# Kernel optimization log

Measured on AMD Instinct MI355X. Metric: run time of the kernel, lower is better.

Reference implementation:

```python
import jax, jax.numpy as jnp
import numpy as np

D_MODEL = 1024
D_FF = 4096


def _layernorm(x, gamma, beta, eps=1e-5):
    mu = jnp.mean(x, axis=-1, keepdims=True)
    var = jnp.var(x, axis=-1, keepdims=True)
    return (x - mu) * jax.lax.rsqrt(var + eps) * gamma + beta


def setup_inputs() -> dict:
    key = jax.random.key(0)
    ks = jax.random.split(key, 7)
    B, S = 4, 2048
    src = jax.random.normal(ks[0], (B, S, D_MODEL), dtype=jnp.float32)
    gamma1 = jnp.ones((D_MODEL,), jnp.float32)
    beta1 = jnp.zeros((D_MODEL,), jnp.float32)
    gamma2 = jnp.ones((D_MODEL,), jnp.float32)
    beta2 = jnp.zeros((D_MODEL,), jnp.float32)
    w1 = jax.random.normal(ks[1], (D_MODEL, D_FF), jnp.float32) * (1.0 / np.sqrt(D_MODEL))
    b1 = jnp.zeros((D_FF,), jnp.float32)
    w2 = jax.random.normal(ks[2], (D_FF, D_MODEL), jnp.float32) * (1.0 / np.sqrt(D_FF))
    b2 = jnp.zeros((D_MODEL,), jnp.float32)
    return {"src": src, "gamma1": gamma1, "beta1": beta1,
            "gamma2": gamma2, "beta2": beta2,
            "w1": w1, "b1": b1, "w2": w2, "b2": b2}


def reference(src, gamma1, beta1, gamma2, beta2, w1, b1, w2, b2):
    # Pre-LN self-attention (single head, Q=K=V=norm_x, no projections)
    norm_x = _layernorm(src, gamma1, beta1)
    dim_k = norm_x.shape[-1]
    scores = jnp.einsum('bqd,bkd->bqk', norm_x, norm_x) / jnp.sqrt(jnp.float32(dim_k))
    weights = jax.nn.softmax(scores, axis=-1)
    attn = jnp.einsum('bqk,bkd->bqd', weights, norm_x)
    x = src + attn  # dropout p=0 -> identity
    # Pre-LN FFN
    h = _layernorm(x, gamma2, beta2)
    h = jax.nn.gelu(h @ w1 + b1, approximate=False)
    h = h @ w2 + b2
    return h + x
```

## Files before the change

kernel.cpp:

```cpp
#include <hip/hip_runtime.h>
#include <hip/hip_bf16.h>
#include <math.h>

typedef __attribute__((ext_vector_type(8))) short s8vec;
typedef __attribute__((ext_vector_type(16))) float f32x16;
typedef __attribute__((ext_vector_type(4))) unsigned short us4;

__device__ __forceinline__ unsigned short f2bf(float f) {
  unsigned u = __float_as_uint(f);
  u = (u + 0x7fffu + ((u >> 16) & 1u)) >> 16;
  return (unsigned short)u;
}
__device__ __forceinline__ float bf2f(unsigned short u) {
  return __uint_as_float(((unsigned)u) << 16);
}

__device__ __forceinline__ float fast_gelu(float t) {
  float t2 = t * t;
  float u = t * (1.59576912f + 0.07135481f * t2);
  float e = __expf(-u);
  return t * __frcp_rn(1.0f + e);
}

__device__ __forceinline__ void async_ld16(const unsigned short* g, unsigned short* l) {
  __builtin_amdgcn_global_load_lds(
      (__attribute__((address_space(1))) void*)g,
      (__attribute__((address_space(3))) void*)l, 16, 0, 0);
}


#define STA(q, tk, bofs) async_ld16(srcA[q] + ((size_t)(tk) << 6), &As[(bofs) + ldsA[q]])
#define STB(j, tk, bofs) async_ld16(srcB[j] + ((size_t)(tk) << 6), &Bs[(bofs) + ldsB[j]])

#define ARD(Q)                                                              \
  _Pragma("unroll") for (int s = 0; s < 4; ++s)                             \
      af[s] = *(const s8vec*)&As[aB + aoff + (Q)*2048 + pc[s]];

#define MFMA_PH(Q)                                                          \
  __builtin_amdgcn_s_barrier();                                             \
  asm volatile("s_waitcnt lgkmcnt(0)" ::: "memory");                        \
  __builtin_amdgcn_sched_barrier(0);                                        \
  __builtin_amdgcn_s_setprio(1);                                            \
  _Pragma("unroll") for (int s = 0; s < 4; ++s) {                           \
    _Pragma("unroll") for (int nf = 0; nf < NF; ++nf)                       \
      acc[Q][nf] = __builtin_amdgcn_mfma_f32_32x32x16_bf16(                 \
          af[s], b[nf][s], acc[Q][nf], 0, 0, 0);                            \
  }                                                                         \
  __builtin_amdgcn_s_setprio(0);

template <int BN, int EPI>
__global__ __launch_bounds__(512, 2) void gemm_nt8(
    const unsigned short* __restrict__ A, const unsigned short* __restrict__ B,
    float* __restrict__ outF, unsigned short* __restrict__ outB,
    const float* __restrict__ bias, const float* __restrict__ res,
    int M, int N, int K,
    long long bA, long long bB, long long bO, long long bR, float scale)
{
  static_assert(BN == 256 || BN == 128, "BN must be 256 or 128");
  constexpr int NB = BN / 64;
  constexpr int NF = BN / 128;
  constexpr int WN = BN / 4;
  constexpr int ABUF = 256 * 64;
  constexpr int BBUF = BN * 64;

  __shared__ __align__(16) unsigned short As[2 * ABUF];
  __shared__ __align__(16) unsigned short Bs[2 * BBUF];

  (void)M;
  const int tid = threadIdx.x;
  const int w = tid >> 6;
  const int l = tid & 63;
  const int z = blockIdx.z;
  A += (size_t)z * bA;
  B += (size_t)z * bB;
  const size_t tileM = (size_t)blockIdx.y * 256;
  const size_t tileN = (size_t)blockIdx.x * BN;

  const int sub = w & 3, half = w >> 2;
  const unsigned short* srcA[4];
  int ldsA[4];
#pragma unroll
  for (int q = 0; q < 4; ++q) {
    const int rb = q * 32 + sub * 8 + half * 128;
    const int r = rb + (l >> 3);
    const int c = (l & 7) ^ (r & 7) ^ ((r >> 3) & 3);
    srcA[q] = A + (tileM + r) * (size_t)K + (c << 3);
    ldsA[q] = rb * 64;
  }
  const unsigned short* srcB[NB];
  int ldsB[NB];
#pragma unroll
  for (int j = 0; j < NB; ++j) {
    const int rb = j * 64 + w * 8;
    const int r = rb + (l >> 3);
    const int c = (l & 7) ^ (r & 7) ^ ((r >> 3) & 3);
    srcB[j] = B + (tileN + r) * (size_t)K + (c << 3);
    ldsB[j] = rb * 64;
  }

  const int wm = half;
  const int wn = sub;
  const int fr = l & 31;
  const int fq = l >> 5;
  const int swz = (l & 7) ^ ((l >> 3) & 3);
  int pc[4];
#pragma unroll
  for (int s = 0; s < 4; ++s) pc[s] = ((((s << 1) + fq) ^ swz) << 3);
  const int aoff = (wm * 128 + fr) * 64;
  int boff[NF];
#pragma unroll
  for (int nf = 0; nf < NF; ++nf) boff[nf] = (wn * WN + nf * 32 + fr) * 64;

  f32x16 acc[4][NF] = {};
  const int NT = K >> 6;

  STA(0, 0, 0); STA(1, 0, 0); STA(2, 0, 0); STA(3, 0, 0);
#pragma unroll
  for (int j = 0; j < NB; ++j) STB(j, 0, 0);
#pragma unroll
  for (int j = 0; j < NB; ++j) STB(j, 1, BBUF);
  STA(0, 1, ABUF); STA(1, 1, ABUF);
  if constexpr (BN == 256) asm volatile("s_waitcnt vmcnt(6)" ::: "memory");
  else                     asm volatile("s_waitcnt vmcnt(4)" ::: "memory");
  __builtin_amdgcn_s_barrier();

  auto tile = [&](int t, int bf) {
    const int aB = bf * ABUF;
    const int bBo = bf * BBUF;
    const int oaB = (bf ^ 1) * ABUF;
    const bool g1 = (t + 1 < NT), g2 = (t + 2 < NT);
    s8vec b[NF][4];
    s8vec af[4];

    ARD(0);
#pragma unroll
    for (int nf = 0; nf < NF; ++nf)
#pragma unroll
      for (int s = 0; s < 4; ++s)
        b[nf][s] = *(const s8vec*)&Bs[bBo + boff[nf] + pc[s]];
    if (g1) { STA(2, t + 1, oaB); STA(3, t + 1, oaB); }
    MFMA_PH(0);
    __builtin_amdgcn_s_barrier();

    ARD(1);
    if (g2) {
      if constexpr (BN == 256) { STB(0, t + 2, bBo); STB(1, t + 2, bBo); }
      else                     { STB(0, t + 2, bBo); }
    }
    MFMA_PH(1);
    __builtin_amdgcn_s_barrier();

    ARD(2);
    if (g2) {
      if constexpr (BN == 256) { STB(2, t + 2, bBo); STB(3, t + 2, bBo); }
      else                     { STB(1, t + 2, bBo); }
    }
    MFMA_PH(2);
    __builtin_amdgcn_s_barrier();

    ARD(3);
    if (g2) { STA(0, t + 2, aB); STA(1, t + 2, aB); }
    MFMA_PH(3);
    if (g2) {
      if constexpr (BN == 256) asm volatile("s_waitcnt vmcnt(6)" ::: "memory");
      else                     asm volatile("s_waitcnt vmcnt(4)" ::: "memory");
    } else {
      asm volatile("s_waitcnt vmcnt(0)" ::: "memory");
    }
    __builtin_amdgcn_s_barrier();
  };

  for (int t = 0; t < NT; t += 2) { tile(t, 0); tile(t + 1, 1); }

  float* oF = outF + (size_t)z * bO;
  unsigned short* oB = outB + (size_t)z * bO;
  const float* rs = res + (size_t)z * bR;

  float bcol[NF];
  if (EPI >= 2) {
#pragma unroll
    for (int nf = 0; nf < NF; ++nf) bcol[nf] = bias[tileN + wn * WN + nf * 32 + fr];
  }

#pragma unroll
  for (int mf = 0; mf < 4; ++mf) {
#pragma unroll
    for (int r = 0; r < 16; ++r) {
      const size_t row = tileM + wm * 128 + (mf << 5) + (r & 3) + ((r >> 2) << 3) + (fq << 2);
      const size_t rb = row * (size_t)N;
#pragma unroll
      for (int nf = 0; nf < NF; ++nf) {
        const size_t col = tileN + wn * WN + (nf << 5) + fr;
        const float v = acc[mf][nf][r];
        if (EPI == 0) {
          oB[rb + col] = f2bf(v * scale);
        } else if (EPI == 1) {
          oF[rb + col] = v + rs[rb + col];
        } else if (EPI == 2) {
          oB[rb + col] = f2bf(fast_gelu(v + bcol[nf]));
        } else {
          oF[rb + col] = v + bcol[nf] + rs[rb + col];
        }
      }
    }
  }
}

__global__ __launch_bounds__(256) void ln_row(
    const float* __restrict__ x, const float* __restrict__ gamma,
    const float* __restrict__ beta, unsigned short* __restrict__ out)
{
  const int row = blockIdx.x;
  const float4* xr = (const float4*)(x + (size_t)row * 1024);
  const int tid = threadIdx.x;
  float4 v = xr[tid];
  float s = v.x + v.y + v.z + v.w;
  float q = v.x * v.x + v.y * v.y + v.z * v.z + v.w * v.w;
#pragma unroll
  for (int off = 32; off > 0; off >>= 1) {
    s += __shfl_down(s, off);
    q += __shfl_down(q, off);
  }
  __shared__ float rs_[4], rq_[4];
  const int w = tid >> 6, l = tid & 63;
  if (l == 0) { rs_[w] = s; rq_[w] = q; }
  __syncthreads();
  s = rs_[0] + rs_[1] + rs_[2] + rs_[3];
  q = rq_[0] + rq_[1] + rq_[2] + rq_[3];
  const float mu = s * (1.0f / 1024.0f);
  const float var = q * (1.0f / 1024.0f) - mu * mu;
  const float rstd = rsqrtf(var + 1e-5f);
  const float4 g = ((const float4*)gamma)[tid];
  const float4 b = ((const float4*)beta)[tid];
  us4 o;
  o.x = f2bf((v.x - mu) * rstd * g.x + b.x);
  o.y = f2bf((v.y - mu) * rstd * g.y + b.y);
  o.z = f2bf((v.z - mu) * rstd * g.z + b.z);
  o.w = f2bf((v.w - mu) * rstd * g.w + b.w);
  ((us4*)(out + (size_t)row * 1024))[tid] = o;
}

__global__ __launch_bounds__(256) void softmax_row(
    const unsigned short* __restrict__ sc, unsigned short* __restrict__ pr)
{
  const int row = blockIdx.x;
  const s8vec* s8 = (const s8vec*)(sc + (size_t)row * 2048);
  const int tid = threadIdx.x;
  s8vec a = s8[tid];
  float x[8];
#pragma unroll
  for (int i = 0; i < 8; ++i) x[i] = bf2f((unsigned short)a[i]);
  float mx = x[0];
#pragma unroll
  for (int i = 1; i < 8; ++i) mx = fmaxf(mx, x[i]);
#pragma unroll
  for (int off = 32; off > 0; off >>= 1) mx = fmaxf(mx, __shfl_down(mx, off));
  __shared__ float red[4];
  const int w = tid >> 6, l = tid & 63;
  if (l == 0) red[w] = mx;
  __syncthreads();
  mx = fmaxf(fmaxf(red[0], red[1]), fmaxf(red[2], red[3]));
  __syncthreads();
  float e[8], s = 0.f;
#pragma unroll
  for (int i = 0; i < 8; ++i) { e[i] = __expf(x[i] - mx); s += e[i]; }
#pragma unroll
  for (int off = 32; off > 0; off >>= 1) s += __shfl_down(s, off);
  if (l == 0) red[w] = s;
  __syncthreads();
  s = red[0] + red[1] + red[2] + red[3];
  const float inv = 1.0f / s;
  s8vec o;
#pragma unroll
  for (int i = 0; i < 8; ++i) o[i] = (short)f2bf(e[i] * inv);
  ((s8vec*)(pr + (size_t)row * 2048))[tid] = o;
}

template <bool BF16IN>
__global__ __launch_bounds__(256) void transpose_conv(
    const void* __restrict__ in_, unsigned short* __restrict__ out,
    int R, int C, long long bIn, long long bOut)
{
  __shared__ float tile[32][33];
  const int z = blockIdx.z;
  const int tx = threadIdx.x, ty = threadIdx.y;
  const int c0 = blockIdx.x * 32, r0 = blockIdx.y * 32;
  if (BF16IN) {
    const unsigned short* in = (const unsigned short*)in_ + (size_t)z * bIn;
    for (int i = ty; i < 32; i += 8)
      tile[i][tx] = bf2f(in[(size_t)(r0 + i) * C + c0 + tx]);
  } else {
    const float* in = (const float*)in_ + (size_t)z * bIn;
    for (int i = ty; i < 32; i += 8)
      tile[i][tx] = in[(size_t)(r0 + i) * C + c0 + tx];
  }
  __syncthreads();
  unsigned short* o = out + (size_t)z * bOut;
  for (int i = ty; i < 32; i += 8)
    o[(size_t)(c0 + i) * R + r0 + tx] = f2bf(tile[tx][i]);
}

extern "C" void kernel_launch(void* const* d_in, const int* in_sizes, int n_in,
                              void* d_out, int out_size, void* d_ws, size_t ws_size,
                              hipStream_t stream)
{
  (void)in_sizes; (void)n_in; (void)out_size; (void)ws_size;
  const float* src = (const float*)d_in[0];
  const float* g1  = (const float*)d_in[1];
  const float* be1 = (const float*)d_in[2];
  const float* g2  = (const float*)d_in[3];
  const float* be2 = (const float*)d_in[4];
  const float* w1  = (const float*)d_in[5];
  const float* b1  = (const float*)d_in[6];
  const float* w2  = (const float*)d_in[7];
  const float* b2  = (const float*)d_in[8];
  float* out = (float*)d_out;

  char* ws = (char*)d_ws;
  const size_t SZ_NORMX  = (size_t)8192 * 1024 * 2;
  const size_t SZ_SCORES = (size_t)4 * 2048 * 2048 * 4;
  const size_t SZ_PROBS  = (size_t)4 * 2048 * 2048 * 2;
  const size_t SZ_X      = (size_t)8192 * 1024 * 4;
  const size_t SZ_W1T    = (size_t)1024 * 4096 * 2;

  unsigned short* normx  = (unsigned short*)(ws);
  unsigned short* normxT = (unsigned short*)(ws + SZ_NORMX);
  unsigned short* scores = (unsigned short*)(ws + 2 * SZ_NORMX);
  unsigned short* probs  = (unsigned short*)(ws + 2 * SZ_NORMX + SZ_SCORES);
  float*          xbuf   = (float*)(ws + 2 * SZ_NORMX + SZ_SCORES + SZ_PROBS);
  unsigned short* w1t    = (unsigned short*)(ws + 2 * SZ_NORMX + SZ_SCORES + SZ_PROBS + SZ_X);
  unsigned short* w2t    = (unsigned short*)(ws + 2 * SZ_NORMX + SZ_SCORES + SZ_PROBS + SZ_X + SZ_W1T);
  unsigned short* normx2 = normx;
  unsigned short* hbuf   = scores;

  const dim3 tb(32, 8);
  transpose_conv<false><<<dim3(128, 32, 1), tb, 0, stream>>>(w1, w1t, 1024, 4096, 0, 0);
  transpose_conv<false><<<dim3(32, 128, 1), tb, 0, stream>>>(w2, w2t, 4096, 1024, 0, 0);

  ln_row<<<8192, 256, 0, stream>>>(src, g1, be1, normx);
  transpose_conv<true><<<dim3(32, 64, 4), tb, 0, stream>>>(
      normx, normxT, 2048, 1024, (long long)2048 * 1024, (long long)1024 * 2048);

  gemm_nt8<256, 0><<<dim3(8, 8, 4), 512, 0, stream>>>(
      normx, normx, nullptr, scores, nullptr, nullptr,
      2048, 2048, 1024,
      (long long)2048 * 1024, (long long)2048 * 1024, (long long)2048 * 2048, 0, 0.03125f);

  softmax_row<<<8192, 256, 0, stream>>>(scores, probs);

  gemm_nt8<128, 1><<<dim3(8, 8, 4), 512, 0, stream>>>(
      probs, normxT, xbuf, nullptr, nullptr, src,
      2048, 1024, 2048,
      (long long)2048 * 2048, (long long)1024 * 2048, (long long)2048 * 1024,
      (long long)2048 * 1024, 1.0f);

  ln_row<<<8192, 256, 0, stream>>>(xbuf, g2, be2, normx2);

  gemm_nt8<256, 2><<<dim3(16, 32, 1), 512, 0, stream>>>(
      normx2, w1t, nullptr, hbuf, b1, nullptr,
      8192, 4096, 1024, 0, 0, 0, 0, 1.0f);

  gemm_nt8<128, 3><<<dim3(8, 32, 1), 512, 0, stream>>>(
      hbuf, w2t, out, nullptr, b2, xbuf,
      8192, 1024, 4096, 0, 0, 0, 0, 1.0f);
}
```

Measured before the change: 429.3 us.

## Remap workgroups across XCDs and restructure BN=128 GEMM loop into two phases

Workgroup indices are remapped so that consecutive tiles land on the same XCD chiplet, to improve L2 locality for shared A/B panels. The BN=128 path now runs two MFMA phases per K-tile, each covering two A fragments, instead of four single-fragment phases. This halves the barriers per K-tile and issues all B and A prefetches together. The remap assumes the grid dims are powers of two and that the workgroup count divides by 8. The new BN=128 schedule also holds more fragments in registers, which may raise register pressure.

```diff
diff --git a/kernel.cpp b/kernel.cpp
--- a/kernel.cpp
+++ b/kernel.cpp
@@ -32,21 +32,15 @@
 #define STA(q, tk, bofs) async_ld16(srcA[q] + ((size_t)(tk) << 6), &As[(bofs) + ldsA[q]])
 #define STB(j, tk, bofs) async_ld16(srcB[j] + ((size_t)(tk) << 6), &Bs[(bofs) + ldsB[j]])
 
-#define ARD(Q)                                                              \
-  _Pragma("unroll") for (int s = 0; s < 4; ++s)                             \
-      af[s] = *(const s8vec*)&As[aB + aoff + (Q)*2048 + pc[s]];
-
-#define MFMA_PH(Q)                                                          \
+#define PH_SYNC_PRE()                                                       \
   __builtin_amdgcn_s_barrier();                                             \
   asm volatile("s_waitcnt lgkmcnt(0)" ::: "memory");                        \
   __builtin_amdgcn_sched_barrier(0);                                        \
-  __builtin_amdgcn_s_setprio(1);                                            \
-  _Pragma("unroll") for (int s = 0; s < 4; ++s) {                           \
-    _Pragma("unroll") for (int nf = 0; nf < NF; ++nf)                       \
-      acc[Q][nf] = __builtin_amdgcn_mfma_f32_32x32x16_bf16(                 \
-          af[s], b[nf][s], acc[Q][nf], 0, 0, 0);                            \
-  }                                                                         \
-  __builtin_amdgcn_s_setprio(0);
+  __builtin_amdgcn_s_setprio(1)
+
+#define PH_SYNC_POST()                                                      \
+  __builtin_amdgcn_s_setprio(0);                                            \
+  __builtin_amdgcn_s_barrier()
 
 template <int BN, int EPI>
 __global__ __launch_bounds__(512, 2) void gemm_nt8(
@@ -70,11 +64,21 @@
   const int tid = threadIdx.x;
   const int w = tid >> 6;
   const int l = tid & 63;
-  const int z = blockIdx.z;
+
+  const unsigned gx = gridDim.x, gy = gridDim.y;
+  unsigned lin = blockIdx.x + gx * (blockIdx.y + gy * blockIdx.z);
+  const unsigned nwg = gx * gy * gridDim.z;
+  lin = (lin & 7u) * (nwg >> 3) + (lin >> 3);
+  const unsigned bx = lin & (gx - 1u);
+  const unsigned tmp = lin >> __builtin_ctz(gx);
+  const unsigned by = tmp & (gy - 1u);
+  const unsigned bz = tmp >> __builtin_ctz(gy);
+
+  const int z = (int)bz;
   A += (size_t)z * bA;
   B += (size_t)z * bB;
-  const size_t tileM = (size_t)blockIdx.y * 256;
-  const size_t tileN = (size_t)blockIdx.x * BN;
+  const size_t tileM = (size_t)by * 256;
+  const size_t tileN = (size_t)bx * BN;
 
   const int sub = w & 3, half = w >> 2;
   const unsigned short* srcA[4];
@@ -114,63 +118,124 @@
   f32x16 acc[4][NF] = {};
   const int NT = K >> 6;
 
-  STA(0, 0, 0); STA(1, 0, 0); STA(2, 0, 0); STA(3, 0, 0);
-#pragma unroll
-  for (int j = 0; j < NB; ++j) STB(j, 0, 0);
-#pragma unroll
-  for (int j = 0; j < NB; ++j) STB(j, 1, BBUF);
-  STA(0, 1, ABUF); STA(1, 1, ABUF);
-  if constexpr (BN == 256) asm volatile("s_waitcnt vmcnt(6)" ::: "memory");
-  else                     asm volatile("s_waitcnt vmcnt(4)" ::: "memory");
-  __builtin_amdgcn_s_barrier();
-
-  auto tile = [&](int t, int bf) {
-    const int aB = bf * ABUF;
-    const int bBo = bf * BBUF;
-    const int oaB = (bf ^ 1) * ABUF;
-    const bool g1 = (t + 1 < NT), g2 = (t + 2 < NT);
-    s8vec b[NF][4];
-    s8vec af[4];
-
-    ARD(0);
-#pragma unroll
-    for (int nf = 0; nf < NF; ++nf)
+  if constexpr (BN == 256) {
+    STA(0, 0, 0); STA(1, 0, 0); STA(2, 0, 0); STA(3, 0, 0);
+#pragma unroll
+    for (int j = 0; j < 4; ++j) STB(j, 0, 0);
+#pragma unroll
+    for (int j = 0; j < 4; ++j) STB(j, 1, BBUF);
+    STA(0, 1, ABUF); STA(1, 1, ABUF);
+    asm volatile("s_waitcnt vmcnt(6)" ::: "memory");
+    __builtin_amdgcn_s_barrier();
+
+    auto tile = [&](int t, int bf) {
+      const int aB = bf * ABUF, bBo = bf * BBUF, oaB = (bf ^ 1) * ABUF;
+      const bool g1 = (t + 1 < NT), g2 = (t + 2 < NT);
+      s8vec b[2][4];
+      s8vec af[4];
+
+#pragma unroll
+      for (int s = 0; s < 4; ++s) af[s] = *(const s8vec*)&As[aB + aoff + 0 * 2048 + pc[s]];
+#pragma unroll
+      for (int nf = 0; nf < 2; ++nf)
+#pragma unroll
+        for (int s = 0; s < 4; ++s)
+          b[nf][s] = *(const s8vec*)&Bs[bBo + boff[nf] + pc[s]];
+      if (g1) { STA(2, t + 1, oaB); STA(3, t + 1, oaB); }
+      PH_SYNC_PRE();
 #pragma unroll
       for (int s = 0; s < 4; ++s)
-        b[nf][s] = *(const s8vec*)&Bs[bBo + boff[nf] + pc[s]];
-    if (g1) { STA(2, t + 1, oaB); STA(3, t + 1, oaB); }
-    MFMA_PH(0);
+#pragma unroll
+        for (int nf = 0; nf < 2; ++nf)
+          acc[0][nf] = __builtin_amdgcn_mfma_f32_32x32x16_bf16(af[s], b[nf][s], acc[0][nf], 0, 0, 0);
+      PH_SYNC_POST();
+
+#pragma unroll
+      for (int s = 0; s < 4; ++s) af[s] = *(const s8vec*)&As[aB + aoff + 1 * 2048 + pc[s]];
+      if (g2) { STB(0, t + 2, bBo); STB(1, t + 2, bBo); }
+      PH_SYNC_PRE();
+#pragma unroll
+      for (int s = 0; s < 4; ++s)
+#pragma unroll
+        for (int nf = 0; nf < 2; ++nf)
+          acc[1][nf] = __builtin_amdgcn_mfma_f32_32x32x16_bf16(af[s], b[nf][s], acc[1][nf], 0, 0, 0);
+      PH_SYNC_POST();
+
+#pragma unroll
+      for (int s = 0; s < 4; ++s) af[s] = *(const s8vec*)&As[aB + aoff + 2 * 2048 + pc[s]];
+      if (g2) { STB(2, t + 2, bBo); STB(3, t + 2, bBo); }
+      PH_SYNC_PRE();
+#pragma unroll
+      for (int s = 0; s < 4; ++s)
+#pragma unroll
+        for (int nf = 0; nf < 2; ++nf)
+          acc[2][nf] = __builtin_amdgcn_mfma_f32_32x32x16_bf16(af[s], b[nf][s], acc[2][nf], 0, 0, 0);
+      PH_SYNC_POST();
+
+#pragma unroll
+      for (int s = 0; s < 4; ++s) af[s] = *(const s8vec*)&As[aB + aoff + 3 * 2048 + pc[s]];
+      if (g2) { STA(0, t + 2, aB); STA(1, t + 2, aB); }
+      PH_SYNC_PRE();
+#pragma unroll
+      for (int s = 0; s < 4; ++s)
+#pragma unroll
+        for (int nf = 0; nf < 2; ++nf)
+          acc[3][nf] = __builtin_amdgcn_mfma_f32_32x32x16_bf16(af[s], b[nf][s], acc[3][nf], 0, 0, 0);
+      __builtin_amdgcn_s_setprio(0);
+      if (g2) asm volatile("s_waitcnt vmcnt(6)" ::: "memory");
+      else    asm volatile("s_waitcnt vmcnt(0)" ::: "memory");
+      __builtin_amdgcn_s_barrier();
+    };
+
+    for (int t = 0; t < NT; t += 2) { tile(t, 0); tile(t + 1, 1); }
+  } else {
+    STA(0, 0, 0); STA(1, 0, 0); STA(2, 0, 0); STA(3, 0, 0);
+    STB(0, 0, 0); STB(1, 0, 0);
+    STB(0, 1, BBUF); STB(1, 1, BBUF);
+    STA(0, 1, ABUF); STA(1, 1, ABUF);
+    asm volatile("s_waitcnt vmcnt(4)" ::: "memory");
     __builtin_amdgcn_s_barrier();
 
-    ARD(1);
-    if (g2) {
-      if constexpr (BN == 256) { STB(0, t + 2, bBo); STB(1, t + 2, bBo); }
-      else                     { STB(0, t + 2, bBo); }
-    }
-    MFMA_PH(1);
-    __builtin_amdgcn_s_barrier();
-
-    ARD(2);
-    if (g2) {
-      if constexpr (BN == 256) { STB(2, t + 2, bBo); STB(3, t + 2, bBo); }
-      else                     { STB(1, t + 2, bBo); }
-    }
-    MFMA_PH(2);
-    __builtin_amdgcn_s_barrier();
-
-    ARD(3);
-    if (g2) { STA(0, t + 2, aB); STA(1, t + 2, aB); }
-    MFMA_PH(3);
-    if (g2) {
-      if constexpr (BN == 256) asm volatile("s_waitcnt vmcnt(6)" ::: "memory");
-      else                     asm volatile("s_waitcnt vmcnt(4)" ::: "memory");
-    } else {
-      asm volatile("s_waitcnt vmcnt(0)" ::: "memory");
-    }
-    __builtin_amdgcn_s_barrier();
-  };
-
-  for (int t = 0; t < NT; t += 2) { tile(t, 0); tile(t + 1, 1); }
+    auto tile = [&](int t, int bf) {
+      const int aB = bf * ABUF, bBo = bf * BBUF, oaB = (bf ^ 1) * ABUF;
+      const bool g1 = (t + 1 < NT), g2 = (t + 2 < NT);
+      s8vec b[4], a0[4], a1[4];
+
+#pragma unroll
+      for (int s = 0; s < 4; ++s) {
+        b[s]  = *(const s8vec*)&Bs[bBo + boff[0] + pc[s]];
+        a0[s] = *(const s8vec*)&As[aB + aoff + 0 * 2048 + pc[s]];
+        a1[s] = *(const s8vec*)&As[aB + aoff + 1 * 2048 + pc[s]];
+      }
+      if (g1) { STA(2, t + 1, oaB); STA(3, t + 1, oaB); }
+      PH_SYNC_PRE();
+#pragma unroll
+      for (int s = 0; s < 4; ++s) {
+        acc[0][0] = __builtin_amdgcn_mfma_f32_32x32x16_bf16(a0[s], b[s], acc[0][0], 0, 0, 0);
+        acc[1][0] = __builtin_amdgcn_mfma_f32_32x32x16_bf16(a1[s], b[s], acc[1][0], 0, 0, 0);
+      }
+      PH_SYNC_POST();
+
+#pragma unroll
+      for (int s = 0; s < 4; ++s) {
+        a0[s] = *(const s8vec*)&As[aB + aoff + 2 * 2048 + pc[s]];
+        a1[s] = *(const s8vec*)&As[aB + aoff + 3 * 2048 + pc[s]];
+      }
+      if (g2) { STB(0, t + 2, bBo); STB(1, t + 2, bBo); STA(0, t + 2, aB); STA(1, t + 2, aB); }
+      PH_SYNC_PRE();
+#pragma unroll
+      for (int s = 0; s < 4; ++s) {
+        acc[2][0] = __builtin_amdgcn_mfma_f32_32x32x16_bf16(a0[s], b[s], acc[2][0], 0, 0, 0);
+        acc[3][0] = __builtin_amdgcn_mfma_f32_32x32x16_bf16(a1[s], b[s], acc[3][0], 0, 0, 0);
+      }
+      __builtin_amdgcn_s_setprio(0);
+      if (g2) asm volatile("s_waitcnt vmcnt(4)" ::: "memory");
+      else    asm volatile("s_waitcnt vmcnt(0)" ::: "memory");
+      __builtin_amdgcn_s_barrier();
+    };
+
+    for (int t = 0; t < NT; t += 2) { tile(t, 0); tile(t + 1, 1); }
+  }
 
   float* oF = outF + (size_t)z * bO;
   unsigned short* oB = outB + (size_t)z * bO;
```

Result: faster. 402.7 us (-6.2%).

## Restructure GEMM main loop into two LDS-read/MFMA phases with XCD-aware block remap

Applied to the files above, without the earlier changes.

Collapses the four per-quarter LDS read/MFMA phases into two larger phases. All B fragments and half the A fragments are loaded up front, and the MFMAs start after a partial lgkmcnt wait, which removes two barriers per k-tile and lets LDS reads overlap with matrix math. Workgroup IDs are also remapped so that consecutive tiles land on the same XCD (stride by 8), aiming for better L2 reuse. Per-row source pointer arrays are replaced by one base pointer plus offsets to cut register use. The larger register footprint risks spills or lower occupancy, and the remap assumes power-of-two grid dimensions.

```diff
diff --git a/kernel.cpp b/kernel.cpp
--- a/kernel.cpp
+++ b/kernel.cpp
@@ -29,24 +29,14 @@
 }
 
 
-#define STA(q, tk, bofs) async_ld16(srcA[q] + ((size_t)(tk) << 6), &As[(bofs) + ldsA[q]])
-#define STB(j, tk, bofs) async_ld16(srcB[j] + ((size_t)(tk) << 6), &Bs[(bofs) + ldsB[j]])
-
-#define ARD(Q)                                                              \
-  _Pragma("unroll") for (int s = 0; s < 4; ++s)                             \
-      af[s] = *(const s8vec*)&As[aB + aoff + (Q)*2048 + pc[s]];
-
-#define MFMA_PH(Q)                                                          \
-  __builtin_amdgcn_s_barrier();                                             \
-  asm volatile("s_waitcnt lgkmcnt(0)" ::: "memory");                        \
-  __builtin_amdgcn_sched_barrier(0);                                        \
-  __builtin_amdgcn_s_setprio(1);                                            \
-  _Pragma("unroll") for (int s = 0; s < 4; ++s) {                           \
-    _Pragma("unroll") for (int nf = 0; nf < NF; ++nf)                       \
-      acc[Q][nf] = __builtin_amdgcn_mfma_f32_32x32x16_bf16(                 \
-          af[s], b[nf][s], acc[Q][nf], 0, 0, 0);                            \
-  }                                                                         \
-  __builtin_amdgcn_s_setprio(0);
+#define STA(q, tk, bofs)                                                    \
+  async_ld16(srcA0 + (size_t)(q) * 32 * K + ((size_t)(tk) << 6),            \
+             &As[(bofs) + ldsA0 + (q) * 2048])
+#define STB(j, tk, bofs)                                                    \
+  async_ld16(srcB0 + (size_t)(j) * 64 * K + ((size_t)(tk) << 6),            \
+             &Bs[(bofs) + ldsB0 + (j) * 4096])
+
+#define SB0() __builtin_amdgcn_sched_barrier(0)
 
 template <int BN, int EPI>
 __global__ __launch_bounds__(512, 2) void gemm_nt8(
@@ -70,33 +60,32 @@
   const int tid = threadIdx.x;
   const int w = tid >> 6;
   const int l = tid & 63;
-  const int z = blockIdx.z;
+
+  const unsigned gx = gridDim.x, gy = gridDim.y;
+  unsigned lin = blockIdx.x + gx * (blockIdx.y + gy * blockIdx.z);
+  const unsigned nwg = gx * gy * gridDim.z;
+  lin = (lin & 7u) * (nwg >> 3) + (lin >> 3);
+  const unsigned bx = lin & (gx - 1u);
+  const unsigned tmp = lin >> __builtin_ctz(gx);
+  const unsigned by = tmp & (gy - 1u);
+  const unsigned bz = tmp >> __builtin_ctz(gy);
+
+  const int z = (int)bz;
   A += (size_t)z * bA;
   B += (size_t)z * bB;
-  const size_t tileM = (size_t)blockIdx.y * 256;
-  const size_t tileN = (size_t)blockIdx.x * BN;
+  const size_t tileM = (size_t)by * 256;
+  const size_t tileN = (size_t)bx * BN;
 
   const int sub = w & 3, half = w >> 2;
-  const unsigned short* srcA[4];
-  int ldsA[4];
-#pragma unroll
-  for (int q = 0; q < 4; ++q) {
-    const int rb = q * 32 + sub * 8 + half * 128;
-    const int r = rb + (l >> 3);
-    const int c = (l & 7) ^ (r & 7) ^ ((r >> 3) & 3);
-    srcA[q] = A + (tileM + r) * (size_t)K + (c << 3);
-    ldsA[q] = rb * 64;
-  }
-  const unsigned short* srcB[NB];
-  int ldsB[NB];
-#pragma unroll
-  for (int j = 0; j < NB; ++j) {
-    const int rb = j * 64 + w * 8;
-    const int r = rb + (l >> 3);
-    const int c = (l & 7) ^ (r & 7) ^ ((r >> 3) & 3);
-    srcB[j] = B + (tileN + r) * (size_t)K + (c << 3);
-    ldsB[j] = rb * 64;
-  }
+  const int rA = sub * 8 + half * 128 + (l >> 3);
+  const int cA = (l & 7) ^ (rA & 7) ^ ((rA >> 3) & 3);
+  const unsigned short* srcA0 = A + (tileM + rA) * (size_t)K + (cA << 3);
+  const int ldsA0 = (sub * 8 + half * 128) * 64;
+
+  const int rB = w * 8 + (l >> 3);
+  const int cB = (l & 7) ^ (rB & 7) ^ ((rB >> 3) & 3);
+  const unsigned short* srcB0 = B + (tileN + rB) * (size_t)K + (cB << 3);
+  const int ldsB0 = (w * 8) * 64;
 
   const int wm = half;
   const int wn = sub;
@@ -120,50 +109,66 @@
 #pragma unroll
   for (int j = 0; j < NB; ++j) STB(j, 1, BBUF);
   STA(0, 1, ABUF); STA(1, 1, ABUF);
-  if constexpr (BN == 256) asm volatile("s_waitcnt vmcnt(6)" ::: "memory");
-  else                     asm volatile("s_waitcnt vmcnt(4)" ::: "memory");
+  if constexpr (NB == 4) asm volatile("s_waitcnt vmcnt(6)" ::: "memory");
+  else                   asm volatile("s_waitcnt vmcnt(4)" ::: "memory");
   __builtin_amdgcn_s_barrier();
 
   auto tile = [&](int t, int bf) {
-    const int aB = bf * ABUF;
-    const int bBo = bf * BBUF;
-    const int oaB = (bf ^ 1) * ABUF;
+    const int aB = bf * ABUF, bBo = bf * BBUF, oaB = (bf ^ 1) * ABUF;
     const bool g1 = (t + 1 < NT), g2 = (t + 2 < NT);
-    s8vec b[NF][4];
-    s8vec af[4];
-
-    ARD(0);
-#pragma unroll
-    for (int nf = 0; nf < NF; ++nf)
-#pragma unroll
-      for (int s = 0; s < 4; ++s)
+    s8vec b[NF][4], aA[2][4], aC[2][4];
+
+#pragma unroll
+    for (int s = 0; s < 4; ++s) {
+#pragma unroll
+      for (int nf = 0; nf < NF; ++nf)
         b[nf][s] = *(const s8vec*)&Bs[bBo + boff[nf] + pc[s]];
+      aA[0][s] = *(const s8vec*)&As[aB + aoff + 0 * 2048 + pc[s]];
+      aA[1][s] = *(const s8vec*)&As[aB + aoff + 1 * 2048 + pc[s]];
+    }
+    SB0();
+#pragma unroll
+    for (int s = 0; s < 4; ++s) {
+      aC[0][s] = *(const s8vec*)&As[aB + aoff + 2 * 2048 + pc[s]];
+      aC[1][s] = *(const s8vec*)&As[aB + aoff + 3 * 2048 + pc[s]];
+    }
     if (g1) { STA(2, t + 1, oaB); STA(3, t + 1, oaB); }
-    MFMA_PH(0);
+    SB0();
+    asm volatile("s_waitcnt lgkmcnt(8)" ::: "memory");
+    SB0();
+    __builtin_amdgcn_s_setprio(1);
+#pragma unroll
+    for (int s = 0; s < 4; ++s)
+#pragma unroll
+      for (int i = 0; i < 2; ++i)
+#pragma unroll
+        for (int nf = 0; nf < NF; ++nf)
+          acc[i][nf] = __builtin_amdgcn_mfma_f32_32x32x16_bf16(aA[i][s], b[nf][s], acc[i][nf], 0, 0, 0);
+    SB0();
+    __builtin_amdgcn_s_setprio(0);
     __builtin_amdgcn_s_barrier();
 
-    ARD(1);
     if (g2) {
-      if constexpr (BN == 256) { STB(0, t + 2, bBo); STB(1, t + 2, bBo); }
-      else                     { STB(0, t + 2, bBo); }
-    }
-    MFMA_PH(1);
-    __builtin_amdgcn_s_barrier();
-
-    ARD(2);
+#pragma unroll
+      for (int j = 0; j < NB; ++j) STB(j, t + 2, bBo);
+      STA(0, t + 2, aB); STA(1, t + 2, aB);
+    }
+    SB0();
+    asm volatile("s_waitcnt lgkmcnt(0)" ::: "memory");
+    SB0();
+    __builtin_amdgcn_s_setprio(1);
+#pragma unroll
+    for (int s = 0; s < 4; ++s)
+#pragma unroll
+      for (int i = 0; i < 2; ++i)
+#pragma unroll
+        for (int nf = 0; nf < NF; ++nf)
+          acc[2 + i][nf] = __builtin_amdgcn_mfma_f32_32x32x16_bf16(aC[i][s], b[nf][s], acc[2 + i][nf], 0, 0, 0);
+    SB0();
+    __builtin_amdgcn_s_setprio(0);
     if (g2) {
-      if constexpr (BN == 256) { STB(2, t + 2, bBo); STB(3, t + 2, bBo); }
-      else                     { STB(1, t + 2, bBo); }
-    }
-    MFMA_PH(2);
-    __builtin_amdgcn_s_barrier();
-
-    ARD(3);
-    if (g2) { STA(0, t + 2, aB); STA(1, t + 2, aB); }
-    MFMA_PH(3);
-    if (g2) {
-      if constexpr (BN == 256) asm volatile("s_waitcnt vmcnt(6)" ::: "memory");
-      else                     asm volatile("s_waitcnt vmcnt(4)" ::: "memory");
+      if constexpr (NB == 4) asm volatile("s_waitcnt vmcnt(6)" ::: "memory");
+      else                   asm volatile("s_waitcnt vmcnt(4)" ::: "memory");
     } else {
       asm volatile("s_waitcnt vmcnt(0)" ::: "memory");
     }
```

Measured after the change: 406.8 us. 1.06x faster.
